# Performance work log

Hardware: AMD Instinct MI355X
Metric: run time of the kernel (lower is better)

## Reference

```python
import jax, jax.numpy as jnp
import numpy as np

D_MODEL = 1024
H = 16
D_K = D_MODEL // H
EPS = 1e-8


def _feature_map(x):
    # elu(x) + 1 (Performer/linear-attention positive feature map)
    return jax.nn.elu(x) + 1.0


def setup_inputs() -> dict:
    key = jax.random.key(0)
    ks = jax.random.split(key, 8)
    B, L = 4, 2048
    q = jax.random.normal(ks[0], (B, L, D_MODEL), dtype=jnp.float32)
    k = jax.random.normal(ks[1], (B, L, D_MODEL), dtype=jnp.float32)
    v = jax.random.normal(ks[2], (B, L, D_MODEL), dtype=jnp.float32)
    mask = jnp.ones((B, 1, 1, L), dtype=bool)
    s = 1.0 / np.sqrt(D_MODEL)
    w_q = jax.random.normal(ks[3], (D_MODEL, D_MODEL), dtype=jnp.float32) * s
    w_k = jax.random.normal(ks[4], (D_MODEL, D_MODEL), dtype=jnp.float32) * s
    w_v = jax.random.normal(ks[5], (D_MODEL, D_MODEL), dtype=jnp.float32) * s
    w_o = jax.random.normal(ks[6], (D_MODEL, D_MODEL), dtype=jnp.float32) * s
    return {"q": q, "k": k, "v": v, "mask": mask,
            "w_q": w_q, "w_k": w_k, "w_v": w_v, "w_o": w_o}


def reference(q, k, v, mask, w_q, w_k, w_v, w_o):
    # Linear (use_Linear=True) branch of MultiHeadAttentionBlock.forward.
    B, Lq, _ = q.shape
    Lk = k.shape[1]
    # fused-style projections (torch Linear: x @ W.T), split into heads -> bhnd
    query = (q @ w_q.T).reshape(B, Lq, H, D_K).transpose(0, 2, 1, 3)
    key_  = (k @ w_k.T).reshape(B, Lk, H, D_K).transpose(0, 2, 1, 3)
    value = (v @ w_v.T).reshape(B, Lk, H, D_K).transpose(0, 2, 1, 3)

    Q = _feature_map(query)            # [B,H,Lq,d_k]
    K = _feature_map(key_)             # [B,H,Lk,d_k]
    KV = jnp.einsum('bhnd,bhnm->bhdm', K, value)           # [B,H,d_k,d_k]
    Z = 1.0 / (jnp.einsum('bhnd,bhd->bhn', Q, K.sum(axis=2)) + EPS)  # [B,H,Lq]
    out = jnp.einsum('bhnd,bhdm,bhn->bhnm', Q, KV, Z)      # [B,H,Lq,d_k]

    out = out.transpose(0, 2, 1, 3).reshape(B, Lq, D_MODEL)
    return out @ w_o.T
```

## Files before the change

kernel.cpp:

```cpp
#include <hip/hip_runtime.h>
#include <cstdint>
#include <cstddef>

typedef __bf16 bf16;
typedef __bf16 bf16x8 __attribute__((ext_vector_type(8)));
typedef __bf16 bf16x4 __attribute__((ext_vector_type(4)));
typedef float  f32x4  __attribute__((ext_vector_type(4)));

#define DM     1024
#define MROWS  8192
#define LSEQ   2048
#define NBATCH 4
#define NHEAD  16
#define BHEADS 64
#define KV_S   8
#define KVT_STRIDE 4160

__device__ __forceinline__ void async16(const void* g, void* l) {
    __builtin_amdgcn_global_load_lds(
        (const __attribute__((address_space(1))) void*)g,
        (__attribute__((address_space(3))) void*)l, 16, 0, 0);
}

struct CastArgs {
    const float* s[7];
    bf16*        d[7];
    int          nblk[7];
};

__global__ __launch_bounds__(256) void cast_all(CastArgs a) {
    const int z = blockIdx.z;
    if ((int)blockIdx.x >= a.nblk[z]) return;
    const int i = blockIdx.x * 256 + threadIdx.x;
    float4 f = ((const float4*)a.s[z])[i];
    bf16x4 o; o[0] = (bf16)f.x; o[1] = (bf16)f.y; o[2] = (bf16)f.z; o[3] = (bf16)f.w;
    ((bf16x4*)a.d[z])[i] = o;
}

struct GemmArgs {
    const bf16* A[3];
    const bf16* B[3];
    void*       C[3];
    int         mode[3];
};

__global__ __launch_bounds__(256) void gemm_nt(GemmArgs args) {
    const int z = blockIdx.z;
    const bf16* __restrict__ A  = args.A[z];
    const bf16* __restrict__ Bm = args.B[z];
    void* Cp = args.C[z];
    const int mode = args.mode[z];
    const int K = DM;

    __shared__ __attribute__((aligned(16))) bf16 sA[128 * 64];
    __shared__ __attribute__((aligned(16))) bf16 sB[128 * 64];

    const int tid  = threadIdx.x;
    const int wave = tid >> 6;
    const int lane = tid & 63;
    const int wm = wave >> 1, wn = wave & 1;

    const int fb = blockIdx.x + 8 * (int)blockIdx.y;
    const int bx = (fb >> 3) & 7;
    const int by = (fb & 7) * 8 + (fb >> 6);
    const int row0 = by * 128;
    const int col0 = bx * 128;

    const int rr = lane >> 3;
    const int cc = lane & 7;
    const int csw = ((cc ^ rr) * 8);
    const bf16* gA = A  + (size_t)(row0 + wave * 32 + rr) * K + csw;
    const bf16* gB = Bm + (size_t)(col0 + wave * 32 + rr) * K + csw;

    f32x4 acc[4][4] = {};

    const int lr = lane & 15;
    const int qd = lane >> 4;
    const int swz = lr & 7;

    for (int k0 = 0; k0 < K; k0 += 64) {
        #pragma unroll
        for (int j = 0; j < 4; ++j) {
            async16(gA + k0 + (size_t)(j * 8) * K, &sA[(wave * 32 + j * 8) * 64]);
            async16(gB + k0 + (size_t)(j * 8) * K, &sB[(wave * 32 + j * 8) * 64]);
        }
        __syncthreads();

        #pragma unroll
        for (int ks = 0; ks < 2; ++ks) {
            bf16x8 af[4], bfr[4];
            #pragma unroll
            for (int mi = 0; mi < 4; ++mi)
                af[mi] = *(const bf16x8*)&sA[(wm * 64 + mi * 16 + lr) * 64 + (((ks * 4 + qd) ^ swz) * 8)];
            #pragma unroll
            for (int ni = 0; ni < 4; ++ni)
                bfr[ni] = *(const bf16x8*)&sB[(wn * 64 + ni * 16 + lr) * 64 + (((ks * 4 + qd) ^ swz) * 8)];
            #pragma unroll
            for (int mi = 0; mi < 4; ++mi)
                #pragma unroll
                for (int ni = 0; ni < 4; ++ni)
                    acc[mi][ni] = __builtin_amdgcn_mfma_f32_16x16x32_bf16(af[mi], bfr[ni], acc[mi][ni], 0, 0, 0);
        }
        __syncthreads();
    }

    if (mode >= 3) {
        #pragma unroll
        for (int mi = 0; mi < 4; ++mi) {
            const int grow0 = row0 + wm * 64 + mi * 16 + qd * 4;
            const int b  = grow0 >> 11;
            const int n0 = grow0 & 2047;
            #pragma unroll
            for (int ni = 0; ni < 4; ++ni) {
                const int gcol = col0 + wn * 64 + ni * 16 + lr;
                const int h = gcol >> 6;
                const int d = gcol & 63;
                bf16x4 o;
                #pragma unroll
                for (int r = 0; r < 4; ++r) {
                    float val = acc[mi][ni][r];
                    if (mode == 4) val = (val > 0.f) ? (val + 1.f) : __expf(val);
                    o[r] = (bf16)val;
                }
                *(bf16x4*)&((bf16*)Cp)[(size_t)((b * 16 + h) * 64 + d) * 2048 + n0] = o;
            }
        }
    } else {
        #pragma unroll
        for (int mi = 0; mi < 4; ++mi) {
            #pragma unroll
            for (int ni = 0; ni < 4; ++ni) {
                #pragma unroll
                for (int r = 0; r < 4; ++r) {
                    const int grow = row0 + wm * 64 + mi * 16 + qd * 4 + r;
                    const int gcol = col0 + wn * 64 + ni * 16 + lr;
                    float val = acc[mi][ni][r];
                    if (mode == 1) val = (val > 0.f) ? (val + 1.f) : __expf(val);
                    ((bf16*)Cp)[(size_t)grow * DM + gcol] = (bf16)val;
                }
            }
        }
    }
}

__global__ __launch_bounds__(256) void gemm_fin(const bf16* __restrict__ A,
                                                const bf16* __restrict__ Bm,
                                                float* __restrict__ C) {
    const int K = DM;
    __shared__ __attribute__((aligned(16))) bf16 sA[128 * 64];
    __shared__ __attribute__((aligned(16))) bf16 sB[64 * 64];

    const int tid  = threadIdx.x;
    const int wave = tid >> 6;
    const int lane = tid & 63;
    const int wm = wave >> 1, wn = wave & 1;

    const int fb = blockIdx.x + 16 * (int)blockIdx.y;
    const int xcd = fb & 7;
    const int g = fb >> 3;
    const int bx = g & 15;
    const int by = xcd * 8 + (g >> 4);
    const int row0 = by * 128;
    const int col0 = bx * 64;

    const int rr = lane >> 3;
    const int cc = lane & 7;
    const int csw = ((cc ^ rr) * 8);
    const bf16* gA = A  + (size_t)(row0 + wave * 32 + rr) * K + csw;
    const bf16* gB = Bm + (size_t)(col0 + wave * 16 + rr) * K + csw;

    f32x4 acc[4][2] = {};

    const int lr = lane & 15;
    const int qd = lane >> 4;
    const int swz = lr & 7;

    for (int k0 = 0; k0 < K; k0 += 64) {
        #pragma unroll
        for (int j = 0; j < 4; ++j)
            async16(gA + k0 + (size_t)(j * 8) * K, &sA[(wave * 32 + j * 8) * 64]);
        #pragma unroll
        for (int j = 0; j < 2; ++j)
            async16(gB + k0 + (size_t)(j * 8) * K, &sB[(wave * 16 + j * 8) * 64]);
        __syncthreads();

        #pragma unroll
        for (int ks = 0; ks < 2; ++ks) {
            bf16x8 af[4], bfr[2];
            #pragma unroll
            for (int mi = 0; mi < 4; ++mi)
                af[mi] = *(const bf16x8*)&sA[(wm * 64 + mi * 16 + lr) * 64 + (((ks * 4 + qd) ^ swz) * 8)];
            #pragma unroll
            for (int ni = 0; ni < 2; ++ni)
                bfr[ni] = *(const bf16x8*)&sB[(wn * 32 + ni * 16 + lr) * 64 + (((ks * 4 + qd) ^ swz) * 8)];
            #pragma unroll
            for (int mi = 0; mi < 4; ++mi)
                #pragma unroll
                for (int ni = 0; ni < 2; ++ni)
                    acc[mi][ni] = __builtin_amdgcn_mfma_f32_16x16x32_bf16(af[mi], bfr[ni], acc[mi][ni], 0, 0, 0);
        }
        __syncthreads();
    }

    #pragma unroll
    for (int mi = 0; mi < 4; ++mi)
        #pragma unroll
        for (int ni = 0; ni < 2; ++ni)
            #pragma unroll
            for (int r = 0; r < 4; ++r) {
                const int grow = row0 + wm * 64 + mi * 16 + qd * 4 + r;
                const int gcol = col0 + wn * 32 + ni * 16 + lr;
                C[(size_t)grow * DM + gcol] = acc[mi][ni][r];
            }
}

__global__ __launch_bounds__(256) void kv_mfma(const bf16* __restrict__ KpT,
                                               const bf16* __restrict__ VpT,
                                               float* __restrict__ KVTp) {
    const int bh = blockIdx.x, s = blockIdx.y;
    const int tid = threadIdx.x, wave = tid >> 6, lane = tid & 63;

    __shared__ __attribute__((aligned(16))) bf16 sVT[64 * 256];
    __shared__ __attribute__((aligned(16))) bf16 sKT[64 * 256];

    const int dd = lane >> 5;
    const int c  = lane & 31;
    #pragma unroll
    for (int j = 0; j < 8; ++j) {
        const int i2 = (wave * 8 + j) * 2;
        const int r  = i2 + dd;
        const int cs = (c ^ (r & 7)) * 8;
        const size_t gofs = (size_t)(bh * 64 + r) * 2048 + s * 256 + cs;
        async16(VpT + gofs, &sVT[i2 * 256]);
        async16(KpT + gofs, &sKT[i2 * 256]);
    }
    __syncthreads();

    const int lr = lane & 15, qd = lane >> 4;
    f32x4 acc[4] = {};
    const int rA = wave * 16 + lr;
    #pragma unroll
    for (int k0 = 0; k0 < 8; ++k0) {
        const int ch = k0 * 4 + qd;
        bf16x8 a = *(const bf16x8*)&sVT[rA * 256 + ((ch ^ (rA & 7)) * 8)];
        #pragma unroll
        for (int ni = 0; ni < 4; ++ni) {
            const int rB = ni * 16 + lr;
            bf16x8 b = *(const bf16x8*)&sKT[rB * 256 + ((ch ^ (rB & 7)) * 8)];
            acc[ni] = __builtin_amdgcn_mfma_f32_16x16x32_bf16(a, b, acc[ni], 0, 0, 0);
        }
    }

    float* outp = &KVTp[(size_t)(bh * KV_S + s) * KVT_STRIDE];
    #pragma unroll
    for (int ni = 0; ni < 4; ++ni)
        #pragma unroll
        for (int r = 0; r < 4; ++r)
            outp[(wave * 16 + qd * 4 + r) * 64 + ni * 16 + lr] = acc[ni][r];

    if (wave == 0) {
        float ks = 0.f;
        #pragma unroll
        for (int c2 = 0; c2 < 32; ++c2) {
            bf16x8 kk = *(const bf16x8*)&sKT[lane * 256 + ((c2 ^ (lane & 7)) * 8)];
            #pragma unroll
            for (int j = 0; j < 8; ++j) ks += (float)kk[j];
        }
        outp[4096 + lane] = ks;
    }
}

__global__ __launch_bounds__(256) void kv_reduce(const float* __restrict__ KVTp,
                                                 bf16* __restrict__ KVT,
                                                 float* __restrict__ Ksum) {
    const int bh = blockIdx.x;
    const int idx = blockIdx.y * 256 + threadIdx.x;
    if (idx >= KVT_STRIDE) return;
    float s = 0.f;
    #pragma unroll
    for (int p = 0; p < KV_S; ++p) s += KVTp[(size_t)(bh * KV_S + p) * KVT_STRIDE + idx];
    if (idx < 4096) KVT[(size_t)bh * 4096 + idx] = (bf16)s;
    else            Ksum[bh * 64 + (idx - 4096)] = s;
}

__global__ __launch_bounds__(256) void attn_out(const bf16* __restrict__ Qp,
                                                const bf16* __restrict__ KVT,
                                                const float* __restrict__ Ksum,
                                                bf16* __restrict__ Ab) {
    const int bh = blockIdx.y;
    const int b = bh >> 4, h = bh & 15;
    const int row0 = blockIdx.x * 128;
    const int tid = threadIdx.x, wave = tid >> 6, lane = tid & 63;

    __shared__ __attribute__((aligned(16))) bf16 sQ[128 * 64];
    __shared__ __attribute__((aligned(16))) bf16 sKV[64 * 64];
    __shared__ float sKs[64];

    const int rr8 = lane >> 3;
    const int cc8 = lane & 7;
    const int csw = ((cc8 ^ rr8) * 8);

    const bf16* qbase = &Qp[(size_t)(b * LSEQ + row0) * DM + h * 64];
    #pragma unroll
    for (int j = 0; j < 4; ++j) {
        const int r0 = wave * 32 + j * 8;
        async16(qbase + (size_t)(r0 + rr8) * DM + csw, &sQ[r0 * 64]);
    }
    const bf16* kvbase = &KVT[(size_t)bh * 4096];
    #pragma unroll
    for (int j = 0; j < 2; ++j) {
        const int r0 = wave * 16 + j * 8;
        async16(kvbase + (r0 + rr8) * 64 + csw, &sKV[r0 * 64]);
    }
    if (tid < 64) sKs[tid] = Ksum[bh * 64 + tid];
    __syncthreads();

    const int zrow = lane >> 1;
    const int dh = lane & 1;
    float zacc = 0.f;
    {
        const bf16* qr = &sQ[(wave * 32 + zrow) * 64];
        #pragma unroll
        for (int c = 0; c < 4; ++c) {
            const int chunk = dh * 4 + c;
            bf16x8 q8 = *(const bf16x8*)&qr[(chunk ^ (zrow & 7)) * 8];
            const float* ksp = &sKs[chunk * 8];
            #pragma unroll
            for (int j = 0; j < 8; ++j) zacc += (float)q8[j] * ksp[j];
        }
    }
    zacc += __shfl_xor(zacc, 1, 64);
    const float zinv = 1.0f / (zacc + 1e-8f);

    f32x4 acc[2][4] = {};
    const int lr = lane & 15, qd = lane >> 4;
    const int swz = lr & 7;
    #pragma unroll
    for (int ks = 0; ks < 2; ++ks) {
        bf16x8 af[2], bfr[4];
        #pragma unroll
        for (int mi = 0; mi < 2; ++mi)
            af[mi] = *(const bf16x8*)&sQ[(wave * 32 + mi * 16 + lr) * 64 + (((ks * 4 + qd) ^ swz) * 8)];
        #pragma unroll
        for (int ni = 0; ni < 4; ++ni)
            bfr[ni] = *(const bf16x8*)&sKV[(ni * 16 + lr) * 64 + (((ks * 4 + qd) ^ swz) * 8)];
        #pragma unroll
        for (int mi = 0; mi < 2; ++mi)
            #pragma unroll
            for (int ni = 0; ni < 4; ++ni)
                acc[mi][ni] = __builtin_amdgcn_mfma_f32_16x16x32_bf16(af[mi], bfr[ni], acc[mi][ni], 0, 0, 0);
    }

    #pragma unroll
    for (int mi = 0; mi < 2; ++mi) {
        #pragma unroll
        for (int rr = 0; rr < 4; ++rr) {
            const int rlocal = mi * 16 + qd * 4 + rr;
            const float zv = __shfl(zinv, rlocal * 2, 64);
            const int nrow = row0 + wave * 32 + rlocal;
            #pragma unroll
            for (int ni = 0; ni < 4; ++ni)
                Ab[(size_t)(b * LSEQ + nrow) * DM + h * 64 + ni * 16 + lr] =
                    (bf16)(acc[mi][ni][rr] * zv);
        }
    }
}

extern "C" void kernel_launch(void* const* d_in, const int* in_sizes, int n_in,
                              void* d_out, int out_size, void* d_ws, size_t ws_size,
                              hipStream_t stream) {
    const float* q  = (const float*)d_in[0];
    const float* k  = (const float*)d_in[1];
    const float* v  = (const float*)d_in[2];
    const float* wq = (const float*)d_in[4];
    const float* wk = (const float*)d_in[5];
    const float* wv = (const float*)d_in[6];
    const float* wo = (const float*)d_in[7];

    char* ws = (char*)d_ws;
    size_t off = 0;
    auto alloc = [&](size_t bytes) -> void* {
        void* p = ws + off;
        off += (bytes + 255) & ~(size_t)255;
        return p;
    };

    bf16* qb   = (bf16*)alloc((size_t)MROWS * DM * 2);
    bf16* kb   = (bf16*)alloc((size_t)MROWS * DM * 2);
    bf16* vb   = (bf16*)alloc((size_t)MROWS * DM * 2);
    bf16* wqb  = (bf16*)alloc((size_t)DM * DM * 2);
    bf16* wkb  = (bf16*)alloc((size_t)DM * DM * 2);
    bf16* wvb  = (bf16*)alloc((size_t)DM * DM * 2);
    bf16* wob  = (bf16*)alloc((size_t)DM * DM * 2);
    bf16* Qp   = (bf16*)alloc((size_t)MROWS * DM * 2);
    bf16* KpT  = (bf16*)alloc((size_t)MROWS * DM * 2);
    bf16* VpT  = (bf16*)alloc((size_t)MROWS * DM * 2);
    bf16* Ab   = (bf16*)alloc((size_t)MROWS * DM * 2);
    float* KVTp = (float*)alloc((size_t)BHEADS * KV_S * KVT_STRIDE * 4);
    bf16* KVT  = (bf16*)alloc((size_t)BHEADS * 4096 * 2);
    float* Ksum = (float*)alloc((size_t)BHEADS * 64 * 4);

    CastArgs ca;
    ca.s[0] = q;  ca.s[1] = k;  ca.s[2] = v;  ca.s[3] = wq; ca.s[4] = wk; ca.s[5] = wv; ca.s[6] = wo;
    ca.d[0] = qb; ca.d[1] = kb; ca.d[2] = vb; ca.d[3] = wqb; ca.d[4] = wkb; ca.d[5] = wvb; ca.d[6] = wob;
    const int nb_big = MROWS * DM / 4 / 256, nb_w = DM * DM / 4 / 256;
    ca.nblk[0] = nb_big; ca.nblk[1] = nb_big; ca.nblk[2] = nb_big;
    ca.nblk[3] = nb_w; ca.nblk[4] = nb_w; ca.nblk[5] = nb_w; ca.nblk[6] = nb_w;
    cast_all<<<dim3(nb_big, 1, 7), 256, 0, stream>>>(ca);

    GemmArgs pa;
    pa.A[0] = qb;  pa.A[1] = kb;  pa.A[2] = vb;
    pa.B[0] = wqb; pa.B[1] = wkb; pa.B[2] = wvb;
    pa.C[0] = Qp;  pa.C[1] = KpT; pa.C[2] = VpT;
    pa.mode[0] = 1; pa.mode[1] = 4; pa.mode[2] = 3;
    gemm_nt<<<dim3(DM / 128, MROWS / 128, 3), 256, 0, stream>>>(pa);

    kv_mfma<<<dim3(BHEADS, KV_S), 256, 0, stream>>>(KpT, VpT, KVTp);
    kv_reduce<<<dim3(BHEADS, (KVT_STRIDE + 255) / 256), 256, 0, stream>>>(KVTp, KVT, Ksum);

    attn_out<<<dim3(LSEQ / 128, BHEADS), 256, 0, stream>>>(Qp, KVT, Ksum, Ab);

    gemm_fin<<<dim3(DM / 64, MROWS / 128), 256, 0, stream>>>(Ab, wob, (float*)d_out);
}
```

Baseline: 264.7 us.

## Fuse KV partial reduction into attn_out, double KV split, grid-stride cast

Drops the separate kv_reduce kernel: each attn_out block now sums the KV and Ksum partials itself while building its shared-memory KV tile. The KV split count goes from 8 to 16, so kv_mfma gets more blocks with smaller LDS tiles. The cast kernel becomes grid-stride with a fixed 1024-block grid, and launch_bounds occupancy hints are added to several kernels. The cost is that every attn_out block (16 per head) re-reads all 16 fp32 partials, which adds redundant global traffic in exchange for one fewer launch.

```diff
diff --git a/kernel.cpp b/kernel.cpp
--- a/kernel.cpp
+++ b/kernel.cpp
@@ -10,10 +10,9 @@
 #define DM     1024
 #define MROWS  8192
 #define LSEQ   2048
-#define NBATCH 4
 #define NHEAD  16
 #define BHEADS 64
-#define KV_S   8
+#define KV_S   16
 #define KVT_STRIDE 4160
 
 __device__ __forceinline__ void async16(const void* g, void* l) {
@@ -25,16 +24,19 @@
 struct CastArgs {
     const float* s[7];
     bf16*        d[7];
-    int          nblk[7];
+    int          n4[7];
 };
 
 __global__ __launch_bounds__(256) void cast_all(CastArgs a) {
     const int z = blockIdx.z;
-    if ((int)blockIdx.x >= a.nblk[z]) return;
-    const int i = blockIdx.x * 256 + threadIdx.x;
-    float4 f = ((const float4*)a.s[z])[i];
-    bf16x4 o; o[0] = (bf16)f.x; o[1] = (bf16)f.y; o[2] = (bf16)f.z; o[3] = (bf16)f.w;
-    ((bf16x4*)a.d[z])[i] = o;
+    const int n4 = a.n4[z];
+    const float* __restrict__ s = a.s[z];
+    bf16* __restrict__ d = a.d[z];
+    for (int i = blockIdx.x * 256 + threadIdx.x; i < n4; i += 1024 * 256) {
+        float4 f = ((const float4*)s)[i];
+        bf16x4 o; o[0] = (bf16)f.x; o[1] = (bf16)f.y; o[2] = (bf16)f.z; o[3] = (bf16)f.w;
+        ((bf16x4*)d)[i] = o;
+    }
 }
 
 struct GemmArgs {
@@ -44,7 +46,7 @@
     int         mode[3];
 };
 
-__global__ __launch_bounds__(256) void gemm_nt(GemmArgs args) {
+__global__ __launch_bounds__(256, 3) void gemm_nt(GemmArgs args) {
     const int z = blockIdx.z;
     const bf16* __restrict__ A  = args.A[z];
     const bf16* __restrict__ Bm = args.B[z];
@@ -143,9 +145,9 @@
     }
 }
 
-__global__ __launch_bounds__(256) void gemm_fin(const bf16* __restrict__ A,
-                                                const bf16* __restrict__ Bm,
-                                                float* __restrict__ C) {
+__global__ __launch_bounds__(256, 4) void gemm_fin(const bf16* __restrict__ A,
+                                                   const bf16* __restrict__ Bm,
+                                                   float* __restrict__ C) {
     const int K = DM;
     __shared__ __attribute__((aligned(16))) bf16 sA[128 * 64];
     __shared__ __attribute__((aligned(16))) bf16 sB[64 * 64];
@@ -214,25 +216,22 @@
             }
 }
 
-__global__ __launch_bounds__(256) void kv_mfma(const bf16* __restrict__ KpT,
-                                               const bf16* __restrict__ VpT,
-                                               float* __restrict__ KVTp) {
+__global__ __launch_bounds__(256, 4) void kv_mfma(const bf16* __restrict__ KpT,
+                                                  const bf16* __restrict__ VpT,
+                                                  float* __restrict__ KVTp) {
     const int bh = blockIdx.x, s = blockIdx.y;
     const int tid = threadIdx.x, wave = tid >> 6, lane = tid & 63;
 
-    __shared__ __attribute__((aligned(16))) bf16 sVT[64 * 256];
-    __shared__ __attribute__((aligned(16))) bf16 sKT[64 * 256];
-
-    const int dd = lane >> 5;
-    const int c  = lane & 31;
-    #pragma unroll
-    for (int j = 0; j < 8; ++j) {
-        const int i2 = (wave * 8 + j) * 2;
-        const int r  = i2 + dd;
-        const int cs = (c ^ (r & 7)) * 8;
-        const size_t gofs = (size_t)(bh * 64 + r) * 2048 + s * 256 + cs;
-        async16(VpT + gofs, &sVT[i2 * 256]);
-        async16(KpT + gofs, &sKT[i2 * 256]);
+    __shared__ __attribute__((aligned(16))) bf16 sVT[64 * 128];
+    __shared__ __attribute__((aligned(16))) bf16 sKT[64 * 128];
+
+    #pragma unroll
+    for (int j = 0; j < 4; ++j) {
+        const int r  = wave * 16 + j * 4 + (lane >> 4);
+        const int cg = (lane & 15) ^ (r & 7);
+        const size_t gofs = (size_t)(bh * 64 + r) * 2048 + s * 128 + cg * 8;
+        async16(VpT + gofs, &sVT[(wave * 16 + j * 4) * 128]);
+        async16(KpT + gofs, &sKT[(wave * 16 + j * 4) * 128]);
     }
     __syncthreads();
 
@@ -240,13 +239,13 @@
     f32x4 acc[4] = {};
     const int rA = wave * 16 + lr;
     #pragma unroll
-    for (int k0 = 0; k0 < 8; ++k0) {
+    for (int k0 = 0; k0 < 4; ++k0) {
         const int ch = k0 * 4 + qd;
-        bf16x8 a = *(const bf16x8*)&sVT[rA * 256 + ((ch ^ (rA & 7)) * 8)];
+        bf16x8 a = *(const bf16x8*)&sVT[rA * 128 + ((ch ^ (rA & 7)) * 8)];
         #pragma unroll
         for (int ni = 0; ni < 4; ++ni) {
             const int rB = ni * 16 + lr;
-            bf16x8 b = *(const bf16x8*)&sKT[rB * 256 + ((ch ^ (rB & 7)) * 8)];
+            bf16x8 b = *(const bf16x8*)&sKT[rB * 128 + ((ch ^ (rB & 7)) * 8)];
             acc[ni] = __builtin_amdgcn_mfma_f32_16x16x32_bf16(a, b, acc[ni], 0, 0, 0);
         }
     }
@@ -261,8 +260,8 @@
     if (wave == 0) {
         float ks = 0.f;
         #pragma unroll
-        for (int c2 = 0; c2 < 32; ++c2) {
-            bf16x8 kk = *(const bf16x8*)&sKT[lane * 256 + ((c2 ^ (lane & 7)) * 8)];
+        for (int c2 = 0; c2 < 16; ++c2) {
+            bf16x8 kk = *(const bf16x8*)&sKT[lane * 128 + ((c2 ^ (lane & 7)) * 8)];
             #pragma unroll
             for (int j = 0; j < 8; ++j) ks += (float)kk[j];
         }
@@ -270,23 +269,9 @@
     }
 }
 
-__global__ __launch_bounds__(256) void kv_reduce(const float* __restrict__ KVTp,
-                                                 bf16* __restrict__ KVT,
-                                                 float* __restrict__ Ksum) {
-    const int bh = blockIdx.x;
-    const int idx = blockIdx.y * 256 + threadIdx.x;
-    if (idx >= KVT_STRIDE) return;
-    float s = 0.f;
-    #pragma unroll
-    for (int p = 0; p < KV_S; ++p) s += KVTp[(size_t)(bh * KV_S + p) * KVT_STRIDE + idx];
-    if (idx < 4096) KVT[(size_t)bh * 4096 + idx] = (bf16)s;
-    else            Ksum[bh * 64 + (idx - 4096)] = s;
-}
-
-__global__ __launch_bounds__(256) void attn_out(const bf16* __restrict__ Qp,
-                                                const bf16* __restrict__ KVT,
-                                                const float* __restrict__ Ksum,
-                                                bf16* __restrict__ Ab) {
+__global__ __launch_bounds__(256, 4) void attn_out(const bf16* __restrict__ Qp,
+                                                   const float* __restrict__ KVTp,
+                                                   bf16* __restrict__ Ab) {
     const int bh = blockIdx.y;
     const int b = bh >> 4, h = bh & 15;
     const int row0 = blockIdx.x * 128;
@@ -306,13 +291,29 @@
         const int r0 = wave * 32 + j * 8;
         async16(qbase + (size_t)(r0 + rr8) * DM + csw, &sQ[r0 * 64]);
     }
-    const bf16* kvbase = &KVT[(size_t)bh * 4096];
-    #pragma unroll
-    for (int j = 0; j < 2; ++j) {
-        const int r0 = wave * 16 + j * 8;
-        async16(kvbase + (r0 + rr8) * 64 + csw, &sKV[r0 * 64]);
-    }
-    if (tid < 64) sKs[tid] = Ksum[bh * 64 + tid];
+
+    const float* pbase = &KVTp[(size_t)bh * KV_S * KVT_STRIDE];
+    #pragma unroll
+    for (int j = 0; j < 4; ++j) {
+        const int idx4 = j * 256 + tid;
+        const int idx  = idx4 * 4;
+        float4 s4 = {0.f, 0.f, 0.f, 0.f};
+        #pragma unroll
+        for (int p = 0; p < KV_S; ++p) {
+            float4 v = *(const float4*)&pbase[(size_t)p * KVT_STRIDE + idx];
+            s4.x += v.x; s4.y += v.y; s4.z += v.z; s4.w += v.w;
+        }
+        const int row = idx >> 6;
+        const int col = idx & 63;
+        bf16x4 o; o[0] = (bf16)s4.x; o[1] = (bf16)s4.y; o[2] = (bf16)s4.z; o[3] = (bf16)s4.w;
+        *(bf16x4*)&sKV[row * 64 + (((col >> 3) ^ (row & 7)) * 8) + (col & 7)] = o;
+    }
+    if (tid < 64) {
+        float ks = 0.f;
+        #pragma unroll
+        for (int p = 0; p < KV_S; ++p) ks += pbase[(size_t)p * KVT_STRIDE + 4096 + tid];
+        sKs[tid] = ks;
+    }
     __syncthreads();
 
     const int zrow = lane >> 1;
@@ -397,16 +398,14 @@
     bf16* VpT  = (bf16*)alloc((size_t)MROWS * DM * 2);
     bf16* Ab   = (bf16*)alloc((size_t)MROWS * DM * 2);
     float* KVTp = (float*)alloc((size_t)BHEADS * KV_S * KVT_STRIDE * 4);
-    bf16* KVT  = (bf16*)alloc((size_t)BHEADS * 4096 * 2);
-    float* Ksum = (float*)alloc((size_t)BHEADS * 64 * 4);
 
     CastArgs ca;
     ca.s[0] = q;  ca.s[1] = k;  ca.s[2] = v;  ca.s[3] = wq; ca.s[4] = wk; ca.s[5] = wv; ca.s[6] = wo;
     ca.d[0] = qb; ca.d[1] = kb; ca.d[2] = vb; ca.d[3] = wqb; ca.d[4] = wkb; ca.d[5] = wvb; ca.d[6] = wob;
-    const int nb_big = MROWS * DM / 4 / 256, nb_w = DM * DM / 4 / 256;
-    ca.nblk[0] = nb_big; ca.nblk[1] = nb_big; ca.nblk[2] = nb_big;
-    ca.nblk[3] = nb_w; ca.nblk[4] = nb_w; ca.nblk[5] = nb_w; ca.nblk[6] = nb_w;
-    cast_all<<<dim3(nb_big, 1, 7), 256, 0, stream>>>(ca);
+    const int n4_big = MROWS * DM / 4, n4_w = DM * DM / 4;
+    ca.n4[0] = n4_big; ca.n4[1] = n4_big; ca.n4[2] = n4_big;
+    ca.n4[3] = n4_w; ca.n4[4] = n4_w; ca.n4[5] = n4_w; ca.n4[6] = n4_w;
+    cast_all<<<dim3(1024, 1, 7), 256, 0, stream>>>(ca);
 
     GemmArgs pa;
     pa.A[0] = qb;  pa.A[1] = kb;  pa.A[2] = vb;
@@ -416,9 +415,8 @@
     gemm_nt<<<dim3(DM / 128, MROWS / 128, 3), 256, 0, stream>>>(pa);
 
     kv_mfma<<<dim3(BHEADS, KV_S), 256, 0, stream>>>(KpT, VpT, KVTp);
-    kv_reduce<<<dim3(BHEADS, (KVT_STRIDE + 255) / 256), 256, 0, stream>>>(KVTp, KVT, Ksum);
-
-    attn_out<<<dim3(LSEQ / 128, BHEADS), 256, 0, stream>>>(Qp, KVT, Ksum, Ab);
+
+    attn_out<<<dim3(LSEQ / 128, BHEADS), 256, 0, stream>>>(Qp, KVTp, Ab);
 
     gemm_fin<<<dim3(DM / 64, MROWS / 128), 256, 0, stream>>>(Ab, wob, (float*)d_out);
 }
```

New measurement: 276.1 us. +4.3%, slower.
